# Kernel tuning notes

Measured on AMD Instinct MI355X. Metric: run time of the kernel, lower is better.

The kernel has to match this reference:

```python
import jax, jax.numpy as jnp
import numpy as np

C = 256   # channels
T = 16    # num_tokens
B = 8     # batch size (number of point clouds)
N = 131072  # total points across batch
EPS = 1e-5


def setup_inputs() -> dict:
    key = jax.random.key(0)
    ks = jax.random.split(key, 12)
    s = 1.0 / np.sqrt(C)
    x_f = jax.random.normal(ks[0], (N, C), jnp.float32)
    batch_ids = jnp.sort(jax.random.randint(ks[1], (N,), 0, B, dtype=jnp.int32))
    mk = lambda k, shp: (jax.random.normal(k, shp, jnp.float32) * s)
    return {
        "x_f": x_f,
        "batch_ids": batch_ids,
        "Wq": mk(ks[2], (C, C)),      # ME q_conv (1x1)
        "Wk": mk(ks[3], (C, T)),      # ME k_conv (1x1), C -> num_tokens
        "Wp": mk(ks[4], (C, C)),      # ME p_conv
        "Wv": mk(ks[5], (C, C)),      # convvalues (Conv1d k=1)
        "Wke": mk(ks[6], (C, C)),     # convkeys
        "Wqe": mk(ks[7], (C, C)),     # convquries
        "Wemb": mk(ks[8], (C, C)),    # embedding1
        "Wt": mk(ks[9], (C, C)),      # T_conv
        "Wtrans": mk(ks[10], (C, C)), # trans_conv
        "bn_gamma": jnp.ones((C,), jnp.float32),
        "bn_beta": jnp.zeros((C,), jnp.float32),
    }


def _conv1d(W, x):
    # Conv1d(C,C,k=1,bias=False): y[b,o,t] = sum_c W[o,c] x[b,c,t]
    return jnp.einsum('oc,bct->bot', W, x)


def reference(x_f, batch_ids, Wq, Wk, Wp, Wv, Wke, Wqe, Wemb, Wt, Wtrans, bn_gamma, bn_beta):
    # ---- point -> token (segment softmax over points within each cloud) ----
    xq = x_f @ Wq                      # [N, C]
    xk = x_f @ Wk                      # [N, T]  logits
    m = jax.ops.segment_max(xk, batch_ids, num_segments=B)     # [B, T]
    e = jnp.exp(xk - m[batch_ids])                              # [N, T]
    z = jax.ops.segment_sum(e, batch_ids, num_segments=B)      # [B, T]
    w = e / z[batch_ids]                                        # [N, T] softmax over points per segment
    # tokens[b,c,t] = sum_{n in b} w[n,t] * xq[n,c]  (loop over small fixed T)
    tokens = jnp.stack(
        [jax.ops.segment_sum(xq * w[:, t:t + 1], batch_ids, num_segments=B) for t in range(T)],
        axis=-1)                                                # [B, C, T]

    # ---- token self-attention ----
    vals = _conv1d(Wv, tokens)
    keys = _conv1d(Wke, tokens)
    qrs = _conv1d(Wqe, tokens)
    vt_map = jax.nn.softmax(jnp.einsum('bct,bcs->bts', keys, qrs), axis=-1)  # [B,T,T]
    T_middle = jnp.einsum('bts,bcs->bct', vt_map, vals)                      # [B,C,T]
    T_out = tokens + _conv1d(Wemb, T_middle)
    T_P = _conv1d(Wt, T_out)                                                 # [B,C,T]

    # ---- token -> point ----
    xp = x_f @ Wp                                                            # [N,C]
    # dm[n,t] = <xp[n,:], T_P[b_n,:,t]>  (gather per token to avoid [N,C,T])
    dm = jnp.stack(
        [jnp.sum(xp * jnp.take(T_P[:, :, t], batch_ids, axis=0), axis=1) for t in range(T)],
        axis=1)                                                              # [N,T]
    dm = jax.nn.softmax(dm, axis=-1)
    df = jnp.zeros_like(xp)
    for t in range(T):
        df = df + dm[:, t:t + 1] * jnp.take(T_P[:, :, t], batch_ids, axis=0)  # [N,C]

    # ---- trans_conv + BatchNorm(train) + ReLU + residual ----
    xr = df @ Wtrans                                                          # [N,C]
    mean = jnp.mean(xr, axis=0)
    var = jnp.var(xr, axis=0)
    y = bn_gamma * (xr - mean) * jax.lax.rsqrt(var + EPS) + bn_beta
    return x_f + jax.nn.relu(y)
```

## Files before the change

kernel.cpp:

```cpp
#include <hip/hip_runtime.h>

#define NP 131072
#define C 256
#define T 16
#define BB 8
constexpr float EPS = 1e-5f;

constexpr int NT       = NP * T;
constexpr int OFF_DM   = 0;
constexpr int OFF_Z    = NT;
constexpr int OFF_S    = OFF_Z + BB * T;
constexpr int OFF_DMP  = OFF_S + BB * T * C;
constexpr int OFF_SSP  = OFF_DMP + 8 * BB * T;
constexpr int OFF_KEYS = OFF_SSP + 8 * C;
constexpr int OFF_QRS  = OFF_KEYS + BB * T * C;
constexpr int OFF_VALS = OFF_QRS + BB * T * C;
constexpr int OFF_TM   = OFF_VALS + BB * T * C;
constexpr int OFF_TP   = OFF_TM + BB * T * C;
constexpr int OFF_U    = OFF_TP + BB * T * C;
constexpr int OFF_V    = OFF_U + BB * T * C;
constexpr int OFF_CMB  = OFF_V + BB * T * C;
constexpr int OFF_BNA  = OFF_CMB + 5 * C * C;
constexpr int OFF_BNB  = OFF_BNA + C;

constexpr int RPB = 64;
constexpr int AB_RPB = 256;
constexpr int ZERO_N = BB * T + BB * T * C + 8 * BB * T + 8 * C;

__device__ inline float reduceScatter64(const float (&a)[64], int lane) {
  float b32[32];
  {
    bool hi = (lane & 32) != 0;
#pragma unroll
    for (int i = 0; i < 32; ++i) {
      float mine = hi ? a[i + 32] : a[i];
      float th   = hi ? a[i]      : a[i + 32];
      b32[i] = mine + __shfl_xor(th, 32);
    }
  }
  float b16[16];
  {
    bool hi = (lane & 16) != 0;
#pragma unroll
    for (int i = 0; i < 16; ++i) {
      float mine = hi ? b32[i + 16] : b32[i];
      float th   = hi ? b32[i]      : b32[i + 16];
      b16[i] = mine + __shfl_xor(th, 16);
    }
  }
  float b8[8];
  {
    bool hi = (lane & 8) != 0;
#pragma unroll
    for (int i = 0; i < 8; ++i) {
      float mine = hi ? b16[i + 8] : b16[i];
      float th   = hi ? b16[i]     : b16[i + 8];
      b8[i] = mine + __shfl_xor(th, 8);
    }
  }
  float b4[4];
  {
    bool hi = (lane & 4) != 0;
#pragma unroll
    for (int i = 0; i < 4; ++i) {
      float mine = hi ? b8[i + 4] : b8[i];
      float th   = hi ? b8[i]     : b8[i + 4];
      b4[i] = mine + __shfl_xor(th, 4);
    }
  }
  float b2[2];
  {
    bool hi = (lane & 2) != 0;
#pragma unroll
    for (int i = 0; i < 2; ++i) {
      float mine = hi ? b4[i + 2] : b4[i];
      float th   = hi ? b4[i]     : b4[i + 2];
      b2[i] = mine + __shfl_xor(th, 2);
    }
  }
  bool hi = (lane & 1) != 0;
  float mine = hi ? b2[1] : b2[0];
  float th   = hi ? b2[0] : b2[1];
  return mine + __shfl_xor(th, 1);
}

__global__ __launch_bounds__(256) void k0_init(float* __restrict__ ws) {
  int i = blockIdx.x * 256 + threadIdx.x;
  if (i < ZERO_N) ws[OFF_Z + i] = 0.f;
}

__device__ inline void s_flush(float4 (&acc)[T], int cur_b, int lane,
                               float* __restrict__ s) {
#pragma unroll
  for (int t = 0; t < T; ++t) {
    float* p = s + ((size_t)cur_b * T + t) * C + 4 * lane;
    atomicAdd(p + 0, acc[t].x);
    atomicAdd(p + 1, acc[t].y);
    atomicAdd(p + 2, acc[t].z);
    atomicAdd(p + 3, acc[t].w);
    acc[t] = make_float4(0.f, 0.f, 0.f, 0.f);
  }
}

__global__ __launch_bounds__(256) void kAB3(const float* __restrict__ xf,
    const int* __restrict__ bids, const float* __restrict__ Wk,
    float* __restrict__ z, float* __restrict__ s) {
  __shared__ float4 wk_sacc[T * 64];
  __shared__ float e_lds[AB_RPB][T];
  __shared__ float zred[4][64];
  __shared__ int bid_lds[AB_RPB];
  float4* wk4 = wk_sacc;
  float* sacc = (float*)wk_sacc;
  const int tid = threadIdx.x;
  const int n0 = blockIdx.x * AB_RPB;
  {
    int t = tid >> 4, q4 = tid & 15;
    for (int k = 0; k < 4; ++k) {
      int q = q4 * 4 + k;
      wk4[t * 64 + q] = make_float4(Wk[(4 * q + 0) * T + t], Wk[(4 * q + 1) * T + t],
                                    Wk[(4 * q + 2) * T + t], Wk[(4 * q + 3) * T + t]);
    }
  }
  if (tid < AB_RPB) bid_lds[tid] = bids[n0 + tid];
  else if (tid < AB_RPB) {}
  for (int i = tid + 256; i < AB_RPB; i += 256) bid_lds[i] = bids[n0 + i];
  __syncthreads();
  const int wave = tid >> 6, lane = tid & 63;
  const int rr = lane >> 4, tt = lane & 15;
  const float4* xf4 = (const float4*)xf;
  const bool blockUni = (bid_lds[0] == bid_lds[AB_RPB - 1]);
  const int WROWS = AB_RPB / 4;

  int cur_b = bid_lds[wave * WROWS + rr];
  float zacc = 0.f;
  float4 acc2[T];
#pragma unroll
  for (int t = 0; t < T; ++t) acc2[t] = make_float4(0.f, 0.f, 0.f, 0.f);
  int cb2 = bid_lds[wave * WROWS];

  for (int stp = 0; stp < WROWS / 4; ++stp) {
    const int rb = wave * WROWS + stp * 4;
    float4 xs[4];
#pragma unroll
    for (int r = 0; r < 4; ++r)
      xs[r] = xf4[(size_t)(n0 + rb + r) * 64 + lane];
    float acc[64];
#pragma unroll
    for (int t = 0; t < T; ++t) {
      float4 w = wk4[t * 64 + lane];
      acc[0 * 16 + t] = xs[0].x * w.x + xs[0].y * w.y + xs[0].z * w.z + xs[0].w * w.w;
      acc[1 * 16 + t] = xs[1].x * w.x + xs[1].y * w.y + xs[1].z * w.z + xs[1].w * w.w;
      acc[2 * 16 + t] = xs[2].x * w.x + xs[2].y * w.y + xs[2].z * w.z + xs[2].w * w.w;
      acc[3 * 16 + t] = xs[3].x * w.x + xs[3].y * w.y + xs[3].z * w.z + xs[3].w * w.w;
    }
    float rv = reduceScatter64(acc, lane);
    float ev = __expf(rv);
    e_lds[rb + rr][tt] = ev;
    if (!blockUni) {
      int b = bid_lds[rb + rr];
      if (b != cur_b) { atomicAdd(&z[cur_b * T + tt], zacc); zacc = 0.f; cur_b = b; }
    }
    zacc += ev;
    bool uni = blockUni || (bid_lds[rb] == cb2 && bid_lds[rb + 3] == cb2);
    if (uni) {
#pragma unroll
      for (int tq = 0; tq < 4; ++tq) {
#pragma unroll
        for (int r = 0; r < 4; ++r) {
          float4 ev4 = ((const float4*)&e_lds[rb + r][0])[tq];
          acc2[tq * 4 + 0].x = fmaf(ev4.x, xs[r].x, acc2[tq * 4 + 0].x);
          acc2[tq * 4 + 0].y = fmaf(ev4.x, xs[r].y, acc2[tq * 4 + 0].y);
          acc2[tq * 4 + 0].z = fmaf(ev4.x, xs[r].z, acc2[tq * 4 + 0].z);
          acc2[tq * 4 + 0].w = fmaf(ev4.x, xs[r].w, acc2[tq * 4 + 0].w);
          acc2[tq * 4 + 1].x = fmaf(ev4.y, xs[r].x, acc2[tq * 4 + 1].x);
          acc2[tq * 4 + 1].y = fmaf(ev4.y, xs[r].y, acc2[tq * 4 + 1].y);
          acc2[tq * 4 + 1].z = fmaf(ev4.y, xs[r].z, acc2[tq * 4 + 1].z);
          acc2[tq * 4 + 1].w = fmaf(ev4.y, xs[r].w, acc2[tq * 4 + 1].w);
          acc2[tq * 4 + 2].x = fmaf(ev4.z, xs[r].x, acc2[tq * 4 + 2].x);
          acc2[tq * 4 + 2].y = fmaf(ev4.z, xs[r].y, acc2[tq * 4 + 2].y);
          acc2[tq * 4 + 2].z = fmaf(ev4.z, xs[r].z, acc2[tq * 4 + 2].z);
          acc2[tq * 4 + 2].w = fmaf(ev4.z, xs[r].w, acc2[tq * 4 + 2].w);
          acc2[tq * 4 + 3].x = fmaf(ev4.w, xs[r].x, acc2[tq * 4 + 3].x);
          acc2[tq * 4 + 3].y = fmaf(ev4.w, xs[r].y, acc2[tq * 4 + 3].y);
          acc2[tq * 4 + 3].z = fmaf(ev4.w, xs[r].z, acc2[tq * 4 + 3].z);
          acc2[tq * 4 + 3].w = fmaf(ev4.w, xs[r].w, acc2[tq * 4 + 3].w);
        }
      }
    } else {
#pragma unroll
      for (int r = 0; r < 4; ++r) {
        int b = bid_lds[rb + r];
        if (b != cb2) { s_flush(acc2, cb2, lane, s); cb2 = b; }
#pragma unroll
        for (int t = 0; t < T; ++t) {
          float ev2 = e_lds[rb + r][t];
          acc2[t].x = fmaf(ev2, xs[r].x, acc2[t].x);
          acc2[t].y = fmaf(ev2, xs[r].y, acc2[t].y);
          acc2[t].z = fmaf(ev2, xs[r].z, acc2[t].z);
          acc2[t].w = fmaf(ev2, xs[r].w, acc2[t].w);
        }
      }
    }
  }
  if (blockUni) zred[wave][lane] = zacc;
  else atomicAdd(&z[cur_b * T + tt], zacc);
  __syncthreads();
  if (blockUni) {
    if (tid < 64) {
      float zt = zred[0][tid] + zred[1][tid] + zred[2][tid] + zred[3][tid];
      zt += __shfl_xor(zt, 16);
      zt += __shfl_xor(zt, 32);
      if (tid < 16) atomicAdd(&z[bid_lds[0] * T + tid], zt);
    }
    for (int i = tid; i < T * C; i += 256) sacc[i] = 0.f;
    __syncthreads();
#pragma unroll
    for (int t = 0; t < T; ++t) {
      float* p = sacc + t * C + 4 * lane;
      atomicAdd(p + 0, acc2[t].x);
      atomicAdd(p + 1, acc2[t].y);
      atomicAdd(p + 2, acc2[t].z);
      atomicAdd(p + 3, acc2[t].w);
    }
    __syncthreads();
    int b0 = bid_lds[0];
    for (int t = 0; t < T; ++t)
      atomicAdd(&s[((size_t)b0 * T + t) * C + tid], sacc[t * C + tid]);
  } else {
    s_flush(acc2, cb2, lane, s);
  }
}

__global__ __launch_bounds__(256) void k4a_cmb(const float* __restrict__ Wv,
    const float* __restrict__ Wke, const float* __restrict__ Wqe,
    const float* __restrict__ Wt, const float* __restrict__ Wemb,
    const float* __restrict__ Wq, float* __restrict__ cmb) {
  int mm = blockIdx.x, r = blockIdx.y;
  const float* A = (mm == 0) ? Wv : (mm == 1) ? Wke : (mm == 2) ? Wqe : Wt;
  const float* Bm = (mm == 4) ? Wemb : Wq;
  bool modeT = (mm == 4);
  __shared__ float a_lds[8 * C];
  int o0 = r * 8;
  for (int i = threadIdx.x; i < 8 * C; i += 256) a_lds[i] = A[o0 * C + i];
  __syncthreads();
  int cp = threadIdx.x;
  float acc[8];
#pragma unroll
  for (int oo = 0; oo < 8; ++oo) acc[oo] = 0.f;
  for (int c = 0; c < C; ++c) {
    float bb = modeT ? Bm[c * C + cp] : Bm[cp * C + c];
#pragma unroll
    for (int oo = 0; oo < 8; ++oo) acc[oo] = fmaf(a_lds[oo * C + c], bb, acc[oo]);
  }
  float* outp = cmb + mm * C * C;
#pragma unroll
  for (int oo = 0; oo < 8; ++oo) outp[(o0 + oo) * C + cp] = acc[oo];
}

__global__ __launch_bounds__(256) void k4b_kqv(const float* __restrict__ cmb,
    const float* __restrict__ s, const float* __restrict__ z,
    float* __restrict__ keys, float* __restrict__ qrs, float* __restrict__ vals) {
  int b = blockIdx.x, mat = blockIdx.y, q = blockIdx.z;
  const int midx0 = (mat == 0) ? 1 : (mat == 1) ? 2 : 0;
  const float* M = cmb + midx0 * C * C;
  float* outp = (mat == 0) ? keys : (mat == 1) ? qrs : vals;
  __shared__ float s_lds[T * C];
  __shared__ float rz[T];
  if (threadIdx.x < T) rz[threadIdx.x] = 1.f / z[b * T + threadIdx.x];
  __syncthreads();
  for (int i = threadIdx.x; i < T * C; i += 256)
    s_lds[i] = s[(size_t)b * T * C + i] * rz[i >> 8];
  __syncthreads();
  int o = q * 64 + (threadIdx.x & 63);
  int tg = threadIdx.x >> 6;
  float acc[4] = {0.f, 0.f, 0.f, 0.f};
  for (int c = 0; c < C; ++c) {
    float m = M[o * C + c];
#pragma unroll
    for (int tt = 0; tt < 4; ++tt) acc[tt] = fmaf(m, s_lds[(tg * 4 + tt) * C + c], acc[tt]);
  }
#pragma unroll
  for (int tt = 0; tt < 4; ++tt)
    outp[((size_t)b * T + tg * 4 + tt) * C + o] = acc[tt];
}

__global__ __launch_bounds__(256) void k4c_att(const float* __restrict__ keys,
    const float* __restrict__ qrs, const float* __restrict__ vals,
    float* __restrict__ tm) {
  int b = blockIdx.x;
  __shared__ float k_lds[T * 257];
  __shared__ float q_lds[T * 257];
  __shared__ float v_lds[T * 257];
  __shared__ float att[T * 17];
  int tid = threadIdx.x;
  for (int i = tid; i < T * C; i += 256) {
    int t = i >> 8, c = i & 255;
    k_lds[t * 257 + c] = keys[((size_t)b * T + t) * C + c];
    q_lds[t * 257 + c] = qrs[((size_t)b * T + t) * C + c];
    v_lds[t * 257 + c] = vals[((size_t)b * T + t) * C + c];
  }
  __syncthreads();
  {
    int t = tid >> 4, s2 = tid & 15;
    float acc = 0.f;
    for (int o = 0; o < C; ++o) acc = fmaf(k_lds[t * 257 + o], q_lds[s2 * 257 + o], acc);
    att[t * 17 + s2] = acc;
  }
  __syncthreads();
  if (tid < T) {
    float m = -1e30f;
    for (int s2 = 0; s2 < T; ++s2) m = fmaxf(m, att[tid * 17 + s2]);
    float sum = 0.f;
    for (int s2 = 0; s2 < T; ++s2) {
      float ee = __expf(att[tid * 17 + s2] - m);
      att[tid * 17 + s2] = ee;
      sum += ee;
    }
    float inv = 1.f / sum;
    for (int s2 = 0; s2 < T; ++s2) att[tid * 17 + s2] *= inv;
  }
  __syncthreads();
  for (int t = 0; t < T; ++t) {
    float acc = 0.f;
#pragma unroll
    for (int s2 = 0; s2 < T; ++s2) acc = fmaf(att[t * 17 + s2], v_lds[s2 * 257 + tid], acc);
    tm[((size_t)b * T + t) * C + tid] = acc;
  }
}

__global__ __launch_bounds__(256) void k4d_tp(const float* __restrict__ cmb,
    const float* __restrict__ s, const float* __restrict__ z,
    const float* __restrict__ tm, float* __restrict__ tp) {
  int b = blockIdx.x, q = blockIdx.y;
  const float* At = cmb + 3 * C * C;
  const float* Ae = cmb + 4 * C * C;
  __shared__ float s_lds[T * C];
  __shared__ float tm_lds[T * C];
  __shared__ float rz[T];
  if (threadIdx.x < T) rz[threadIdx.x] = 1.f / z[b * T + threadIdx.x];
  __syncthreads();
  for (int i = threadIdx.x; i < T * C; i += 256) {
    s_lds[i] = s[(size_t)b * T * C + i] * rz[i >> 8];
    tm_lds[i] = tm[(size_t)b * T * C + i];
  }
  __syncthreads();
  int o = q * 64 + (threadIdx.x & 63);
  int tg = threadIdx.x >> 6;
  float acc[4] = {0.f, 0.f, 0.f, 0.f};
  for (int c = 0; c < C; ++c) {
    float a1 = At[o * C + c], a2 = Ae[o * C + c];
#pragma unroll
    for (int tt = 0; tt < 4; ++tt) {
      int t = tg * 4 + tt;
      acc[tt] = fmaf(a1, s_lds[t * C + c], fmaf(a2, tm_lds[t * C + c], acc[tt]));
    }
  }
#pragma unroll
  for (int tt = 0; tt < 4; ++tt)
    tp[((size_t)b * T + tg * 4 + tt) * C + o] = acc[tt];
}

__global__ __launch_bounds__(256) void k4e_uv(const float* __restrict__ Wp,
    const float* __restrict__ Wtrans, const float* __restrict__ tp,
    float* __restrict__ u, float* __restrict__ v) {
  int b = blockIdx.x, mat = blockIdx.y, q = blockIdx.z;
  __shared__ float tp_lds[T * C];
  for (int i = threadIdx.x; i < T * C; i += 256) tp_lds[i] = tp[(size_t)b * T * C + i];
  __syncthreads();
  int o = q * 64 + (threadIdx.x & 63);
  int tg = threadIdx.x >> 6;
  float acc[4] = {0.f, 0.f, 0.f, 0.f};
  for (int c = 0; c < C; ++c) {
    float w = mat ? Wtrans[c * C + o] : Wp[o * C + c];
#pragma unroll
    for (int tt = 0; tt < 4; ++tt) acc[tt] = fmaf(w, tp_lds[(tg * 4 + tt) * C + c], acc[tt]);
  }
  float* outp = mat ? v : u;
#pragma unroll
  for (int tt = 0; tt < 4; ++tt)
    outp[((size_t)b * T + tg * 4 + tt) * C + o] = acc[tt];
}

__global__ __launch_bounds__(256) void kDE(const float* __restrict__ xf,
    const int* __restrict__ bids, const float* __restrict__ u,
    const float* __restrict__ v, float* __restrict__ dmo,
    float* __restrict__ dmsum_p, float* __restrict__ sumsq_p) {
  __shared__ float4 u4[T * 64];
  __shared__ float4 v4[T * 64];
  __shared__ float4 ss4[4][64];
  __shared__ float zred[4][64];
  __shared__ int bid_lds[RPB];
  const int tid = threadIdx.x;
  const int n0 = blockIdx.x * RPB;
  const int b0 = bids[n0];
  const int part = blockIdx.x & 7;
  for (int i = tid; i < T * 64; i += 256) {
    u4[i] = ((const float4*)(u + (size_t)b0 * T * C))[i];
    v4[i] = ((const float4*)(v + (size_t)b0 * T * C))[i];
  }
  if (tid < RPB) bid_lds[tid] = bids[n0 + tid];
  __syncthreads();
  const int wave = tid >> 6, lane = tid & 63;
  const int rr = lane >> 4, tt = lane & 15;
  const float4* xf4 = (const float4*)xf;
  const bool blockUni = (bid_lds[0] == bid_lds[RPB - 1]);
  float4 sqacc = make_float4(0.f, 0.f, 0.f, 0.f);
  float dmacc = 0.f;
  int cur_b = bid_lds[wave * 16 + rr];
  for (int stp = 0; stp < 4; ++stp) {
    const int rb = wave * 16 + stp * 4;
    float4 x0 = xf4[(size_t)(n0 + rb + 0) * 64 + lane];
    float4 x1 = xf4[(size_t)(n0 + rb + 1) * 64 + lane];
    float4 x2 = xf4[(size_t)(n0 + rb + 2) * 64 + lane];
    float4 x3 = xf4[(size_t)(n0 + rb + 3) * 64 + lane];
    float acc[64];
    bool fast = blockUni || ((bid_lds[rb] == b0) && (bid_lds[rb + 3] == b0));
    if (fast) {
#pragma unroll
      for (int t = 0; t < T; ++t) {
        float4 w = u4[t * 64 + lane];
        acc[0 * 16 + t] = x0.x * w.x + x0.y * w.y + x0.z * w.z + x0.w * w.w;
        acc[1 * 16 + t] = x1.x * w.x + x1.y * w.y + x1.z * w.z + x1.w * w.w;
        acc[2 * 16 + t] = x2.x * w.x + x2.y * w.y + x2.z * w.z + x2.w * w.w;
        acc[3 * 16 + t] = x3.x * w.x + x3.y * w.y + x3.z * w.z + x3.w * w.w;
      }
    } else {
      int br0 = bid_lds[rb + 0], br1 = bid_lds[rb + 1];
      int br2 = bid_lds[rb + 2], br3 = bid_lds[rb + 3];
#pragma unroll
      for (int t = 0; t < T; ++t) {
        float4 w0 = ((const float4*)(u + ((size_t)br0 * T + t) * C))[lane];
        float4 w1 = ((const float4*)(u + ((size_t)br1 * T + t) * C))[lane];
        float4 w2 = ((const float4*)(u + ((size_t)br2 * T + t) * C))[lane];
        float4 w3 = ((const float4*)(u + ((size_t)br3 * T + t) * C))[lane];
        acc[0 * 16 + t] = x0.x * w0.x + x0.y * w0.y + x0.z * w0.z + x0.w * w0.w;
        acc[1 * 16 + t] = x1.x * w1.x + x1.y * w1.y + x1.z * w1.z + x1.w * w1.w;
        acc[2 * 16 + t] = x2.x * w2.x + x2.y * w2.y + x2.z * w2.z + x2.w * w2.w;
        acc[3 * 16 + t] = x3.x * w3.x + x3.y * w3.y + x3.z * w3.z + x3.w * w3.w;
      }
    }
    float S = reduceScatter64(acc, lane);
    float mx = S;
#pragma unroll
    for (int m = 1; m < 16; m <<= 1) mx = fmaxf(mx, __shfl_xor(mx, m));
    float ev = __expf(S - mx);
    float sm = ev;
#pragma unroll
    for (int m = 1; m < 16; m <<= 1) sm += __shfl_xor(sm, m);
    float dmv = ev / sm;
    int row = n0 + rb + rr;
    dmo[(size_t)row * T + tt] = dmv;
    if (!blockUni) {
      int b = bid_lds[rb + rr];
      if (b != cur_b) { atomicAdd(&dmsum_p[part * BB * T + cur_b * T + tt], dmacc); dmacc = 0.f; cur_b = b; }
    }
    dmacc += dmv;
#pragma unroll
    for (int r = 0; r < 4; ++r) {
      int br = blockUni ? b0 : bid_lds[rb + r];
      float4 xr = make_float4(0.f, 0.f, 0.f, 0.f);
      if (br == b0) {
#pragma unroll
        for (int t = 0; t < T; ++t) {
          float d = __shfl(dmv, r * 16 + t);
          float4 vv = v4[t * 64 + lane];
          xr.x = fmaf(d, vv.x, xr.x); xr.y = fmaf(d, vv.y, xr.y);
          xr.z = fmaf(d, vv.z, xr.z); xr.w = fmaf(d, vv.w, xr.w);
        }
      } else {
#pragma unroll
        for (int t = 0; t < T; ++t) {
          float d = __shfl(dmv, r * 16 + t);
          float4 vv = ((const float4*)(v + ((size_t)br * T + t) * C))[lane];
          xr.x = fmaf(d, vv.x, xr.x); xr.y = fmaf(d, vv.y, xr.y);
          xr.z = fmaf(d, vv.z, xr.z); xr.w = fmaf(d, vv.w, xr.w);
        }
      }
      sqacc.x = fmaf(xr.x, xr.x, sqacc.x); sqacc.y = fmaf(xr.y, xr.y, sqacc.y);
      sqacc.z = fmaf(xr.z, xr.z, sqacc.z); sqacc.w = fmaf(xr.w, xr.w, sqacc.w);
    }
  }
  if (blockUni) zred[wave][lane] = dmacc;
  else atomicAdd(&dmsum_p[part * BB * T + cur_b * T + tt], dmacc);
  ss4[wave][lane] = sqacc;
  __syncthreads();
  if (blockUni && tid < 64) {
    float zt = zred[0][tid] + zred[1][tid] + zred[2][tid] + zred[3][tid];
    zt += __shfl_xor(zt, 16);
    zt += __shfl_xor(zt, 32);
    if (tid < 16) atomicAdd(&dmsum_p[part * BB * T + b0 * T + tid], zt);
  }
  {
    int l = tid >> 2, k = tid & 3;
    float vsum = ((const float*)&ss4[0][l])[k] + ((const float*)&ss4[1][l])[k] +
                 ((const float*)&ss4[2][l])[k] + ((const float*)&ss4[3][l])[k];
    atomicAdd(&sumsq_p[part * C + tid], vsum);
  }
}

__global__ __launch_bounds__(256) void k7_bn(const float* __restrict__ dmsum_p,
    const float* __restrict__ sumsq_p, const float* __restrict__ v,
    const float* __restrict__ gamma, const float* __restrict__ beta,
    float* __restrict__ bn_a, float* __restrict__ bn_b) {
  int o = threadIdx.x;
  float mean = 0.f;
  for (int i = 0; i < BB * T; ++i) {
    float ds = 0.f;
#pragma unroll
    for (int p = 0; p < 8; ++p) ds += dmsum_p[p * BB * T + i];
    mean = fmaf(ds, v[(size_t)i * C + o], mean);
  }
  mean *= (1.f / NP);
  float ss = 0.f;
#pragma unroll
  for (int p = 0; p < 8; ++p) ss += sumsq_p[p * C + o];
  float var = ss * (1.f / NP) - mean * mean;
  float a = gamma[o] * rsqrtf(var + EPS);
  bn_a[o] = a;
  bn_b[o] = beta[o] - a * mean;
}

__global__ __launch_bounds__(256) void kF_out(const float* __restrict__ xf,
    const int* __restrict__ bids, const float* __restrict__ dm,
    const float* __restrict__ v, const float* __restrict__ bn_a,
    const float* __restrict__ bn_b, float* __restrict__ out) {
  __shared__ float4 v4[T * 64];
  __shared__ float dm_lds[RPB][17];
  __shared__ int bid_lds[RPB];
  const int tid = threadIdx.x;
  const int n0 = blockIdx.x * RPB;
  const int b0 = bids[n0];
  for (int i = tid; i < T * 64; i += 256)
    v4[i] = ((const float4*)(v + (size_t)b0 * T * C))[i];
  {
    float4 d4 = ((const float4*)(dm + (size_t)n0 * T))[tid];
    int r = tid >> 2, c0 = (4 * tid) & 15;
    dm_lds[r][c0] = d4.x; dm_lds[r][c0 + 1] = d4.y;
    dm_lds[r][c0 + 2] = d4.z; dm_lds[r][c0 + 3] = d4.w;
  }
  if (tid < RPB) bid_lds[tid] = bids[n0 + tid];
  __syncthreads();
  const int wave = tid >> 6, lane = tid & 63;
  float4 a4 = ((const float4*)bn_a)[lane];
  float4 b4 = ((const float4*)bn_b)[lane];
  const float4* xf4 = (const float4*)xf;
  float4* out4 = (float4*)out;
  for (int stp = 0; stp < 4; ++stp) {
    const int rb = wave * 16 + stp * 4;
    float4 x0 = xf4[(size_t)(n0 + rb + 0) * 64 + lane];
    float4 x1 = xf4[(size_t)(n0 + rb + 1) * 64 + lane];
    float4 x2 = xf4[(size_t)(n0 + rb + 2) * 64 + lane];
    float4 x3 = xf4[(size_t)(n0 + rb + 3) * 64 + lane];
    float4 acc0 = {0, 0, 0, 0}, acc1 = {0, 0, 0, 0}, acc2 = {0, 0, 0, 0}, acc3 = {0, 0, 0, 0};
    bool fast = (bid_lds[rb] == b0) && (bid_lds[rb + 3] == b0);
    if (fast) {
#pragma unroll
      for (int t = 0; t < T; ++t) {
        float4 vv = v4[t * 64 + lane];
        float d0 = dm_lds[rb + 0][t], d1 = dm_lds[rb + 1][t];
        float d2 = dm_lds[rb + 2][t], d3 = dm_lds[rb + 3][t];
        acc0.x = fmaf(d0, vv.x, acc0.x); acc0.y = fmaf(d0, vv.y, acc0.y);
        acc0.z = fmaf(d0, vv.z, acc0.z); acc0.w = fmaf(d0, vv.w, acc0.w);
        acc1.x = fmaf(d1, vv.x, acc1.x); acc1.y = fmaf(d1, vv.y, acc1.y);
        acc1.z = fmaf(d1, vv.z, acc1.z); acc1.w = fmaf(d1, vv.w, acc1.w);
        acc2.x = fmaf(d2, vv.x, acc2.x); acc2.y = fmaf(d2, vv.y, acc2.y);
        acc2.z = fmaf(d2, vv.z, acc2.z); acc2.w = fmaf(d2, vv.w, acc2.w);
        acc3.x = fmaf(d3, vv.x, acc3.x); acc3.y = fmaf(d3, vv.y, acc3.y);
        acc3.z = fmaf(d3, vv.z, acc3.z); acc3.w = fmaf(d3, vv.w, acc3.w);
      }
    } else {
      int br0 = bid_lds[rb + 0], br1 = bid_lds[rb + 1];
      int br2 = bid_lds[rb + 2], br3 = bid_lds[rb + 3];
#pragma unroll
      for (int t = 0; t < T; ++t) {
        float4 v0 = ((const float4*)(v + ((size_t)br0 * T + t) * C))[lane];
        float4 v1 = ((const float4*)(v + ((size_t)br1 * T + t) * C))[lane];
        float4 v2 = ((const float4*)(v + ((size_t)br2 * T + t) * C))[lane];
        float4 v3 = ((const float4*)(v + ((size_t)br3 * T + t) * C))[lane];
        float d0 = dm_lds[rb + 0][t], d1 = dm_lds[rb + 1][t];
        float d2 = dm_lds[rb + 2][t], d3 = dm_lds[rb + 3][t];
        acc0.x = fmaf(d0, v0.x, acc0.x); acc0.y = fmaf(d0, v0.y, acc0.y);
        acc0.z = fmaf(d0, v0.z, acc0.z); acc0.w = fmaf(d0, v0.w, acc0.w);
        acc1.x = fmaf(d1, v1.x, acc1.x); acc1.y = fmaf(d1, v1.y, acc1.y);
        acc1.z = fmaf(d1, v1.z, acc1.z); acc1.w = fmaf(d1, v1.w, acc1.w);
        acc2.x = fmaf(d2, v2.x, acc2.x); acc2.y = fmaf(d2, v2.y, acc2.y);
        acc2.z = fmaf(d2, v2.z, acc2.z); acc2.w = fmaf(d2, v2.w, acc2.w);
        acc3.x = fmaf(d3, v3.x, acc3.x); acc3.y = fmaf(d3, v3.y, acc3.y);
        acc3.z = fmaf(d3, v3.z, acc3.z); acc3.w = fmaf(d3, v3.w, acc3.w);
      }
    }
    float4 y;
    y.x = x0.x + fmaxf(fmaf(a4.x, acc0.x, b4.x), 0.f);
    y.y = x0.y + fmaxf(fmaf(a4.y, acc0.y, b4.y), 0.f);
    y.z = x0.z + fmaxf(fmaf(a4.z, acc0.z, b4.z), 0.f);
    y.w = x0.w + fmaxf(fmaf(a4.w, acc0.w, b4.w), 0.f);
    out4[(size_t)(n0 + rb + 0) * 64 + lane] = y;
    y.x = x1.x + fmaxf(fmaf(a4.x, acc1.x, b4.x), 0.f);
    y.y = x1.y + fmaxf(fmaf(a4.y, acc1.y, b4.y), 0.f);
    y.z = x1.z + fmaxf(fmaf(a4.z, acc1.z, b4.z), 0.f);
    y.w = x1.w + fmaxf(fmaf(a4.w, acc1.w, b4.w), 0.f);
    out4[(size_t)(n0 + rb + 1) * 64 + lane] = y;
    y.x = x2.x + fmaxf(fmaf(a4.x, acc2.x, b4.x), 0.f);
    y.y = x2.y + fmaxf(fmaf(a4.y, acc2.y, b4.y), 0.f);
    y.z = x2.z + fmaxf(fmaf(a4.z, acc2.z, b4.z), 0.f);
    y.w = x2.w + fmaxf(fmaf(a4.w, acc2.w, b4.w), 0.f);
    out4[(size_t)(n0 + rb + 2) * 64 + lane] = y;
    y.x = x3.x + fmaxf(fmaf(a4.x, acc3.x, b4.x), 0.f);
    y.y = x3.y + fmaxf(fmaf(a4.y, acc3.y, b4.y), 0.f);
    y.z = x3.z + fmaxf(fmaf(a4.z, acc3.z, b4.z), 0.f);
    y.w = x3.w + fmaxf(fmaf(a4.w, acc3.w, b4.w), 0.f);
    out4[(size_t)(n0 + rb + 3) * 64 + lane] = y;
  }
}

extern "C" void kernel_launch(void* const* d_in, const int* in_sizes, int n_in,
                              void* d_out, int out_size, void* d_ws, size_t ws_size,
                              hipStream_t stream) {
  const float* xf    = (const float*)d_in[0];
  const int* bids    = (const int*)d_in[1];
  const float* Wq    = (const float*)d_in[2];
  const float* Wk    = (const float*)d_in[3];
  const float* Wp    = (const float*)d_in[4];
  const float* Wv    = (const float*)d_in[5];
  const float* Wke   = (const float*)d_in[6];
  const float* Wqe   = (const float*)d_in[7];
  const float* Wemb  = (const float*)d_in[8];
  const float* Wt    = (const float*)d_in[9];
  const float* Wtr   = (const float*)d_in[10];
  const float* gamma = (const float*)d_in[11];
  const float* beta  = (const float*)d_in[12];
  float* out = (float*)d_out;
  float* ws  = (float*)d_ws;

  float* dm    = ws + OFF_DM;
  float* z     = ws + OFF_Z;
  float* s     = ws + OFF_S;
  float* dmp   = ws + OFF_DMP;
  float* ssp   = ws + OFF_SSP;
  float* keys  = ws + OFF_KEYS;
  float* qrs   = ws + OFF_QRS;
  float* vals  = ws + OFF_VALS;
  float* tm    = ws + OFF_TM;
  float* tp    = ws + OFF_TP;
  float* u     = ws + OFF_U;
  float* v     = ws + OFF_V;
  float* cmb   = ws + OFF_CMB;
  float* bn_a  = ws + OFF_BNA;
  float* bn_b  = ws + OFF_BNB;

  k0_init<<<(ZERO_N + 255) / 256, 256, 0, stream>>>(ws);
  kAB3<<<NP / AB_RPB, 256, 0, stream>>>(xf, bids, Wk, z, s);
  k4a_cmb<<<dim3(5, 32), 256, 0, stream>>>(Wv, Wke, Wqe, Wt, Wemb, Wq, cmb);
  k4b_kqv<<<dim3(BB, 3, 4), 256, 0, stream>>>(cmb, s, z, keys, qrs, vals);
  k4c_att<<<BB, 256, 0, stream>>>(keys, qrs, vals, tm);
  k4d_tp<<<dim3(BB, 4), 256, 0, stream>>>(cmb, s, z, tm, tp);
  k4e_uv<<<dim3(BB, 2, 4), 256, 0, stream>>>(Wp, Wtr, tp, u, v);
  kDE<<<NP / RPB, 256, 0, stream>>>(xf, bids, u, v, dm, dmp, ssp);
  k7_bn<<<1, 256, 0, stream>>>(dmp, ssp, v, gamma, beta, bn_a, bn_b);
  kF_out<<<NP / RPB, 256, 0, stream>>>(xf, bids, dm, v, bn_a, bn_b, out);
}
```

Before: 345.4 us.

## Fuse token attention chain into one per-batch kernel

Merges the four small token-stage kernels (k/q/v projection, attention, T_P, u/v projection) into a single kernel with one block per batch. Intermediates stay in shared memory instead of going through global buffers, which removes three launches and their round-trips. The trade-off is far less parallelism: only 8 blocks now run, and each thread does all 16 tokens serially over 256 channels with large register arrays. The Wk LDS fill loop in kAB3 is also rewritten into a simpler strided loop.

```diff
diff --git a/kernel.cpp b/kernel.cpp
--- a/kernel.cpp
+++ b/kernel.cpp
@@ -12,12 +12,7 @@
 constexpr int OFF_S    = OFF_Z + BB * T;
 constexpr int OFF_DMP  = OFF_S + BB * T * C;
 constexpr int OFF_SSP  = OFF_DMP + 8 * BB * T;
-constexpr int OFF_KEYS = OFF_SSP + 8 * C;
-constexpr int OFF_QRS  = OFF_KEYS + BB * T * C;
-constexpr int OFF_VALS = OFF_QRS + BB * T * C;
-constexpr int OFF_TM   = OFF_VALS + BB * T * C;
-constexpr int OFF_TP   = OFF_TM + BB * T * C;
-constexpr int OFF_U    = OFF_TP + BB * T * C;
+constexpr int OFF_U    = OFF_SSP + 8 * C;
 constexpr int OFF_V    = OFF_U + BB * T * C;
 constexpr int OFF_CMB  = OFF_V + BB * T * C;
 constexpr int OFF_BNA  = OFF_CMB + 5 * C * C;
@@ -113,17 +108,12 @@
   float* sacc = (float*)wk_sacc;
   const int tid = threadIdx.x;
   const int n0 = blockIdx.x * AB_RPB;
-  {
-    int t = tid >> 4, q4 = tid & 15;
-    for (int k = 0; k < 4; ++k) {
-      int q = q4 * 4 + k;
-      wk4[t * 64 + q] = make_float4(Wk[(4 * q + 0) * T + t], Wk[(4 * q + 1) * T + t],
-                                    Wk[(4 * q + 2) * T + t], Wk[(4 * q + 3) * T + t]);
-    }
-  }
-  if (tid < AB_RPB) bid_lds[tid] = bids[n0 + tid];
-  else if (tid < AB_RPB) {}
-  for (int i = tid + 256; i < AB_RPB; i += 256) bid_lds[i] = bids[n0 + i];
+  for (int i = tid; i < T * 64; i += 256) {
+    int t = i >> 6, q = i & 63;
+    wk4[i] = make_float4(Wk[(4 * q + 0) * T + t], Wk[(4 * q + 1) * T + t],
+                         Wk[(4 * q + 2) * T + t], Wk[(4 * q + 3) * T + t]);
+  }
+  for (int i = tid; i < AB_RPB; i += 256) bid_lds[i] = bids[n0 + i];
   __syncthreads();
   const int wave = tid >> 6, lane = tid & 63;
   const int rr = lane >> 4, tt = lane & 15;
@@ -257,54 +247,51 @@
   for (int oo = 0; oo < 8; ++oo) outp[(o0 + oo) * C + cp] = acc[oo];
 }
 
-__global__ __launch_bounds__(256) void k4b_kqv(const float* __restrict__ cmb,
+__global__ __launch_bounds__(256) void k4all(const float* __restrict__ cmb,
     const float* __restrict__ s, const float* __restrict__ z,
-    float* __restrict__ keys, float* __restrict__ qrs, float* __restrict__ vals) {
-  int b = blockIdx.x, mat = blockIdx.y, q = blockIdx.z;
-  const int midx0 = (mat == 0) ? 1 : (mat == 1) ? 2 : 0;
-  const float* M = cmb + midx0 * C * C;
-  float* outp = (mat == 0) ? keys : (mat == 1) ? qrs : vals;
+    const float* __restrict__ Wp, const float* __restrict__ Wtr,
+    float* __restrict__ u, float* __restrict__ v) {
+  const int b = blockIdx.x;
   __shared__ float s_lds[T * C];
+  __shared__ float bufA[T * 257];
+  __shared__ float bufB[T * 257];
+  __shared__ float att[T * 17];
   __shared__ float rz[T];
-  if (threadIdx.x < T) rz[threadIdx.x] = 1.f / z[b * T + threadIdx.x];
-  __syncthreads();
-  for (int i = threadIdx.x; i < T * C; i += 256)
+  const int tid = threadIdx.x;
+  if (tid < T) rz[tid] = 1.f / z[b * T + tid];
+  __syncthreads();
+  for (int i = tid; i < T * C; i += 256)
     s_lds[i] = s[(size_t)b * T * C + i] * rz[i >> 8];
   __syncthreads();
-  int o = q * 64 + (threadIdx.x & 63);
-  int tg = threadIdx.x >> 6;
-  float acc[4] = {0.f, 0.f, 0.f, 0.f};
-  for (int c = 0; c < C; ++c) {
-    float m = M[o * C + c];
-#pragma unroll
-    for (int tt = 0; tt < 4; ++tt) acc[tt] = fmaf(m, s_lds[(tg * 4 + tt) * C + c], acc[tt]);
-  }
-#pragma unroll
-  for (int tt = 0; tt < 4; ++tt)
-    outp[((size_t)b * T + tg * 4 + tt) * C + o] = acc[tt];
-}
-
-__global__ __launch_bounds__(256) void k4c_att(const float* __restrict__ keys,
-    const float* __restrict__ qrs, const float* __restrict__ vals,
-    float* __restrict__ tm) {
-  int b = blockIdx.x;
-  __shared__ float k_lds[T * 257];
-  __shared__ float q_lds[T * 257];
-  __shared__ float v_lds[T * 257];
-  __shared__ float att[T * 17];
-  int tid = threadIdx.x;
-  for (int i = tid; i < T * C; i += 256) {
-    int t = i >> 8, c = i & 255;
-    k_lds[t * 257 + c] = keys[((size_t)b * T + t) * C + c];
-    q_lds[t * 257 + c] = qrs[((size_t)b * T + t) * C + c];
-    v_lds[t * 257 + c] = vals[((size_t)b * T + t) * C + c];
+  const float* Vc = cmb + 0 * C * C;
+  const float* Kc = cmb + 1 * C * C;
+  const float* Qc = cmb + 2 * C * C;
+  const float* At = cmb + 3 * C * C;
+  const float* Ae = cmb + 4 * C * C;
+  const int o = tid;
+  {
+    float aK[T], aQ[T];
+#pragma unroll
+    for (int t = 0; t < T; ++t) { aK[t] = 0.f; aQ[t] = 0.f; }
+    for (int c = 0; c < C; ++c) {
+      float mk = Kc[o * C + c], mq = Qc[o * C + c];
+#pragma unroll
+      for (int t = 0; t < T; ++t) {
+        float sv = s_lds[t * C + c];
+        aK[t] = fmaf(mk, sv, aK[t]);
+        aQ[t] = fmaf(mq, sv, aQ[t]);
+      }
+    }
+#pragma unroll
+    for (int t = 0; t < T; ++t) { bufA[t * 257 + o] = aK[t]; bufB[t * 257 + o] = aQ[t]; }
   }
   __syncthreads();
   {
     int t = tid >> 4, s2 = tid & 15;
-    float acc = 0.f;
-    for (int o = 0; o < C; ++o) acc = fmaf(k_lds[t * 257 + o], q_lds[s2 * 257 + o], acc);
-    att[t * 17 + s2] = acc;
+    float a = 0.f;
+    for (int oo = 0; oo < C; ++oo)
+      a = fmaf(bufA[t * 257 + oo], bufB[s2 * 257 + oo], a);
+    att[t * 17 + s2] = a;
   }
   __syncthreads();
   if (tid < T) {
@@ -320,65 +307,70 @@
     for (int s2 = 0; s2 < T; ++s2) att[tid * 17 + s2] *= inv;
   }
   __syncthreads();
-  for (int t = 0; t < T; ++t) {
-    float acc = 0.f;
-#pragma unroll
-    for (int s2 = 0; s2 < T; ++s2) acc = fmaf(att[t * 17 + s2], v_lds[s2 * 257 + tid], acc);
-    tm[((size_t)b * T + t) * C + tid] = acc;
-  }
-}
-
-__global__ __launch_bounds__(256) void k4d_tp(const float* __restrict__ cmb,
-    const float* __restrict__ s, const float* __restrict__ z,
-    const float* __restrict__ tm, float* __restrict__ tp) {
-  int b = blockIdx.x, q = blockIdx.y;
-  const float* At = cmb + 3 * C * C;
-  const float* Ae = cmb + 4 * C * C;
-  __shared__ float s_lds[T * C];
-  __shared__ float tm_lds[T * C];
-  __shared__ float rz[T];
-  if (threadIdx.x < T) rz[threadIdx.x] = 1.f / z[b * T + threadIdx.x];
-  __syncthreads();
-  for (int i = threadIdx.x; i < T * C; i += 256) {
-    s_lds[i] = s[(size_t)b * T * C + i] * rz[i >> 8];
-    tm_lds[i] = tm[(size_t)b * T * C + i];
-  }
-  __syncthreads();
-  int o = q * 64 + (threadIdx.x & 63);
-  int tg = threadIdx.x >> 6;
-  float acc[4] = {0.f, 0.f, 0.f, 0.f};
-  for (int c = 0; c < C; ++c) {
-    float a1 = At[o * C + c], a2 = Ae[o * C + c];
-#pragma unroll
-    for (int tt = 0; tt < 4; ++tt) {
-      int t = tg * 4 + tt;
-      acc[tt] = fmaf(a1, s_lds[t * C + c], fmaf(a2, tm_lds[t * C + c], acc[tt]));
-    }
-  }
-#pragma unroll
-  for (int tt = 0; tt < 4; ++tt)
-    tp[((size_t)b * T + tg * 4 + tt) * C + o] = acc[tt];
-}
-
-__global__ __launch_bounds__(256) void k4e_uv(const float* __restrict__ Wp,
-    const float* __restrict__ Wtrans, const float* __restrict__ tp,
-    float* __restrict__ u, float* __restrict__ v) {
-  int b = blockIdx.x, mat = blockIdx.y, q = blockIdx.z;
-  __shared__ float tp_lds[T * C];
-  for (int i = threadIdx.x; i < T * C; i += 256) tp_lds[i] = tp[(size_t)b * T * C + i];
-  __syncthreads();
-  int o = q * 64 + (threadIdx.x & 63);
-  int tg = threadIdx.x >> 6;
-  float acc[4] = {0.f, 0.f, 0.f, 0.f};
-  for (int c = 0; c < C; ++c) {
-    float w = mat ? Wtrans[c * C + o] : Wp[o * C + c];
-#pragma unroll
-    for (int tt = 0; tt < 4; ++tt) acc[tt] = fmaf(w, tp_lds[(tg * 4 + tt) * C + c], acc[tt]);
-  }
-  float* outp = mat ? v : u;
-#pragma unroll
-  for (int tt = 0; tt < 4; ++tt)
-    outp[((size_t)b * T + tg * 4 + tt) * C + o] = acc[tt];
+  {
+    float aV[T];
+#pragma unroll
+    for (int t = 0; t < T; ++t) aV[t] = 0.f;
+    for (int c = 0; c < C; ++c) {
+      float mv = Vc[o * C + c];
+#pragma unroll
+      for (int t = 0; t < T; ++t) aV[t] = fmaf(mv, s_lds[t * C + c], aV[t]);
+    }
+    __syncthreads();
+#pragma unroll
+    for (int t = 0; t < T; ++t) bufA[t * 257 + o] = aV[t];
+  }
+  __syncthreads();
+  {
+    float tmv[T];
+#pragma unroll
+    for (int t = 0; t < T; ++t) {
+      float a = 0.f;
+#pragma unroll
+      for (int s2 = 0; s2 < T; ++s2)
+        a = fmaf(att[t * 17 + s2], bufA[s2 * 257 + tid], a);
+      tmv[t] = a;
+    }
+    __syncthreads();
+#pragma unroll
+    for (int t = 0; t < T; ++t) bufB[t * 257 + tid] = tmv[t];
+  }
+  __syncthreads();
+  {
+    float acc[T];
+#pragma unroll
+    for (int t = 0; t < T; ++t) acc[t] = 0.f;
+    for (int c = 0; c < C; ++c) {
+      float a1 = At[o * C + c], a2 = Ae[o * C + c];
+#pragma unroll
+      for (int t = 0; t < T; ++t)
+        acc[t] = fmaf(a1, s_lds[t * C + c], fmaf(a2, bufB[t * 257 + c], acc[t]));
+    }
+    __syncthreads();
+#pragma unroll
+    for (int t = 0; t < T; ++t) bufA[t * 257 + o] = acc[t];
+  }
+  __syncthreads();
+  {
+    float au[T], av[T];
+#pragma unroll
+    for (int t = 0; t < T; ++t) { au[t] = 0.f; av[t] = 0.f; }
+    for (int c = 0; c < C; ++c) {
+      float wp = Wp[o * C + c];
+      float wt = Wtr[c * C + o];
+#pragma unroll
+      for (int t = 0; t < T; ++t) {
+        float tv = bufA[t * 257 + c];
+        au[t] = fmaf(wp, tv, au[t]);
+        av[t] = fmaf(wt, tv, av[t]);
+      }
+    }
+#pragma unroll
+    for (int t = 0; t < T; ++t) {
+      u[((size_t)b * T + t) * C + o] = au[t];
+      v[((size_t)b * T + t) * C + o] = av[t];
+    }
+  }
 }
 
 __global__ __launch_bounds__(256) void kDE(const float* __restrict__ xf,
@@ -637,11 +629,6 @@
   float* s     = ws + OFF_S;
   float* dmp   = ws + OFF_DMP;
   float* ssp   = ws + OFF_SSP;
-  float* keys  = ws + OFF_KEYS;
-  float* qrs   = ws + OFF_QRS;
-  float* vals  = ws + OFF_VALS;
-  float* tm    = ws + OFF_TM;
-  float* tp    = ws + OFF_TP;
   float* u     = ws + OFF_U;
   float* v     = ws + OFF_V;
   float* cmb   = ws + OFF_CMB;
@@ -651,10 +638,7 @@
   k0_init<<<(ZERO_N + 255) / 256, 256, 0, stream>>>(ws);
   kAB3<<<NP / AB_RPB, 256, 0, stream>>>(xf, bids, Wk, z, s);
   k4a_cmb<<<dim3(5, 32), 256, 0, stream>>>(Wv, Wke, Wqe, Wt, Wemb, Wq, cmb);
-  k4b_kqv<<<dim3(BB, 3, 4), 256, 0, stream>>>(cmb, s, z, keys, qrs, vals);
-  k4c_att<<<BB, 256, 0, stream>>>(keys, qrs, vals, tm);
-  k4d_tp<<<dim3(BB, 4), 256, 0, stream>>>(cmb, s, z, tm, tp);
-  k4e_uv<<<dim3(BB, 2, 4), 256, 0, stream>>>(Wp, Wtr, tp, u, v);
+  k4all<<<BB, 256, 0, stream>>>(cmb, s, z, Wp, Wtr, u, v);
   kDE<<<NP / RPB, 256, 0, stream>>>(xf, bids, u, v, dm, dmp, ssp);
   k7_bn<<<1, 256, 0, stream>>>(dmp, ssp, v, gamma, beta, bn_a, bn_b);
   kF_out<<<NP / RPB, 256, 0, stream>>>(xf, bids, dm, v, bn_a, bn_b, out);
```

New measurement: 420.9 us. +21.8%, slower.
